# Optimization experiments

Measured on AMD Instinct MI355X. Metric: run time of the kernel, lower is better.

## Reference

```python
import jax, jax.numpy as jnp
import numpy as np

B, S, E, H = 4, 2048, 1024, 16
D = E // H  # head_dim = 64
ROPE_BASE = 10000.0


def _rope(x):
    # x: [B, H, S, D] -> rotary position embedding applied over seq dim
    seq_len = x.shape[2]
    inv_freq = 1.0 / (ROPE_BASE ** (jnp.arange(0, D, 2, dtype=jnp.float32) / D))  # [D/2]
    freqs = jnp.arange(seq_len, dtype=jnp.float32)[:, None] * inv_freq[None, :]   # [S, D/2]
    emb = jnp.concatenate([freqs, freqs], axis=-1)                                 # [S, D]
    cos = jnp.cos(emb).astype(x.dtype)
    sin = jnp.sin(emb).astype(x.dtype)
    x1, x2 = jnp.split(x, 2, axis=-1)
    rotated = jnp.concatenate([-x2, x1], axis=-1)
    return x * cos + rotated * sin


def setup_inputs() -> dict:
    key = jax.random.key(0)
    ks = jax.random.split(key, 10)
    p = 0.02
    return {
        "x": jax.random.normal(ks[0], (B, S, E), dtype=jnp.float32),
        "Wq": jax.random.normal(ks[1], (E, E), dtype=jnp.float32) * p,
        "bq": jnp.zeros((E,), dtype=jnp.float32),
        "Wk": jax.random.normal(ks[2], (E, E), dtype=jnp.float32) * p,
        "bk": jnp.zeros((E,), dtype=jnp.float32),
        "Wv": jax.random.normal(ks[3], (E, E), dtype=jnp.float32) * p,
        "bv": jnp.zeros((E,), dtype=jnp.float32),
        "Wo": jax.random.normal(ks[4], (E, E), dtype=jnp.float32) * p,
        "bo": jnp.zeros((E,), dtype=jnp.float32),
        "key_padding_mask": jnp.zeros((B, S), dtype=bool),
    }


def reference(x, Wq, bq, Wk, bk, Wv, bv, Wo, bo, key_padding_mask):
    b, s, _ = x.shape
    # QKV projections -> [B, H, S, D]
    def proj(W, bias):
        return (x @ W + bias).reshape(b, s, H, D).transpose(0, 2, 1, 3)
    q = _rope(proj(Wq, bq))
    k = _rope(proj(Wk, bk))
    v = proj(Wv, bv)
    scale = D ** -0.5
    scores = jnp.einsum('bhqd,bhkd->bhqk', q, k) * scale  # [B, H, S, S]
    scores = jnp.where(key_padding_mask[:, None, None, :], jnp.finfo(scores.dtype).min, scores)
    probs = jax.nn.softmax(scores, axis=-1)
    out = jnp.einsum('bhqk,bhkd->bhqd', probs, v)         # [B, H, S, D]
    out = out.transpose(0, 2, 1, 3).reshape(b, s, E)
    return out @ Wo + bo
```

## Files before the change

### kernel.cpp

```cpp
#include <hip/hip_runtime.h>
#include <hip/hip_bf16.h>
#include <math.h>

#define Bn 4
#define Sn 2048
#define En 1024
#define Hn 16
#define Dn 64
#define Mn (Bn * Sn)

typedef __attribute__((ext_vector_type(8))) short short8;
typedef __attribute__((ext_vector_type(4))) short short4v;
typedef __attribute__((ext_vector_type(4))) float f32x4;
typedef __attribute__((ext_vector_type(16))) float f32x16;
typedef __attribute__((ext_vector_type(2))) unsigned int uint2v;

#if __has_builtin(__builtin_amdgcn_exp2f)
#define EXP2(x) __builtin_amdgcn_exp2f(x)
#else
#define EXP2(x) exp2f(x)
#endif

#if __has_builtin(__builtin_amdgcn_permlane32_swap)
#define HAVE_PLSWAP 1
#endif

#define GLOAD16(g, s) __builtin_amdgcn_global_load_lds( \
    (const __attribute__((address_space(1))) unsigned int*)(g), \
    (__attribute__((address_space(3))) unsigned int*)(s), 16, 0, 0)

__device__ inline unsigned short f2bf(float f) {
    unsigned int u = __float_as_uint(f);
    u += 0x7FFFu + ((u >> 16) & 1u);
    return (unsigned short)(u >> 16);
}
__device__ inline float bf2f(unsigned short h) {
    return __uint_as_float(((unsigned int)h) << 16);
}
__device__ inline short8 ld8s(const unsigned short* p) {
    union { short4v h[2]; short8 v; } r;
    r.h[0] = *(const short4v*)p;
    r.h[1] = *(const short4v*)(p + 4);
    return r.v;
}
__device__ inline short8 g8(const unsigned short* p) {
    union { int4 i; short8 v; } r;
    r.i = *(const int4*)p;
    return r.v;
}

__device__ inline void st16(unsigned short* base, int row, int col16, int4 v) {
    const unsigned off = ((unsigned)(row * 128 + col16 * 2)) ^ ((unsigned)((row & 7) << 4));
    *(int4*)((char*)base + off) = v;
}
__device__ inline short8 ld16(const unsigned short* base, int row, int col16) {
    const unsigned off = ((unsigned)(row * 128 + col16 * 2)) ^ ((unsigned)((row & 7) << 4));
    union { int4 i; short8 v; } r;
    r.i = *(const int4*)((const char*)base + off);
    return r.v;
}

__global__ __launch_bounds__(256) void prep_kernel(
    const float* __restrict__ X, unsigned short* __restrict__ Xh,
    const float* __restrict__ Wq, const float* __restrict__ Wk,
    const float* __restrict__ Wv, const float* __restrict__ Wo,
    unsigned short* __restrict__ WqkvT, unsigned short* __restrict__ WoT,
    float* __restrict__ ct, float* __restrict__ st) {
    const int m = blockIdx.z;
    const int t = threadIdx.x;
    if (m >= 5) {
        const int i = ((m - 5) * 256 + blockIdx.y * 16 + blockIdx.x) * 256 + t;
        float4 v = ((const float4*)X)[i];
        float f[4] = {v.x, v.y, v.z, v.w};
        short4v h;
#pragma unroll
        for (int j = 0; j < 4; ++j) h[j] = (short)f2bf(f[j]);
        ((short4v*)Xh)[i] = h;
        return;
    }
    if (m == 4) {
        const int i = (blockIdx.y * 16 + blockIdx.x) * 256 + t;
        const int s = i >> 5, p = i & 31;
        double inv = pow(10000.0, -(double)p / 32.0);
        double a = (double)s * inv;
        ct[i] = (float)cos(a);
        st[i] = (float)sin(a);
        return;
    }
    const float* W = (m == 0) ? Wq : (m == 1) ? Wk : (m == 2) ? Wv : Wo;
    unsigned short* dst = (m < 3) ? WqkvT + (size_t)m * En * En : WoT;

    __shared__ float Ws[64][65];
    const int kb = blockIdx.y * 64, nb = blockIdx.x * 64;
    const int lr = t >> 2, lc = (t & 3) * 16;
#pragma unroll
    for (int u = 0; u < 4; ++u) {
        float4 v = *(const float4*)&W[(size_t)(kb + lr) * En + nb + lc + 4 * u];
        Ws[lr][lc + 4 * u + 0] = v.x; Ws[lr][lc + 4 * u + 1] = v.y;
        Ws[lr][lc + 4 * u + 2] = v.z; Ws[lr][lc + 4 * u + 3] = v.w;
    }
    __syncthreads();
    const int orow = t >> 2, ock = (t & 3) * 16;
#pragma unroll
    for (int u = 0; u < 4; ++u) {
        short4v hs;
#pragma unroll
        for (int j = 0; j < 4; ++j) hs[j] = (short)f2bf(Ws[ock + 4 * u + j][orow]);
        *(short4v*)&dst[(size_t)(nb + orow) * En + kb + ock + 4 * u] = hs;
    }
}

template <int KN>
__global__ __launch_bounds__(256, 4) void gemm97(
    const unsigned short* __restrict__ A, const unsigned short* __restrict__ Bt,
    const float* __restrict__ b0, const float* __restrict__ bkv,
    const float* __restrict__ bvv,
    unsigned short* __restrict__ oQ, unsigned short* __restrict__ oK,
    unsigned short* __restrict__ oV,
    const float* __restrict__ ct, const float* __restrict__ st) {
    __shared__ __align__(16) unsigned short shmem[17408];
    unsigned short (*As)[64] = (unsigned short(*)[64])&shmem[0];
    unsigned short (*Bs)[64] = (unsigned short(*)[64])&shmem[8192];
    const int t = threadIdx.x;
    const int w = t >> 6, l = t & 63;
    const int wm = w & 1, wn = w >> 1;
    const int q = l >> 4, ln16 = l & 15;
    const int r8 = l >> 3, i8 = l & 7;

    int bx = blockIdx.x, by = blockIdx.y;
    {
        const int gx = gridDim.x;
        const int nwg = gx * gridDim.y;
        if ((nwg & 7) == 0) {
            const int n = by * gx + bx;
            const int s = (n & 7) * (nwg >> 3) + (n >> 3);
            bx = s % gx; by = s / gx;
        }
    }
    const int m0 = by * 128, n0 = bx * 128;

    f32x4 acc[4][4];
#pragma unroll
    for (int i = 0; i < 4; ++i)
#pragma unroll
        for (int j = 0; j < 4; ++j)
#pragma unroll
            for (int r = 0; r < 4; ++r) acc[i][j][r] = 0.0f;

    const unsigned short* Ag = &A[(size_t)(m0 + 32 * w + r8) * KN + 8 * i8];
    const unsigned short* Bg = &Bt[(size_t)(n0 + 32 * w + r8) * KN + 8 * i8];

    for (int k0 = 0; k0 < KN; k0 += 64) {
        __syncthreads();
#pragma unroll
        for (int j = 0; j < 4; ++j) {
            GLOAD16(Ag + (size_t)(8 * j) * KN + k0, &As[32 * w + 8 * j][0]);
            GLOAD16(Bg + (size_t)(8 * j) * KN + k0, &Bs[32 * w + 8 * j][0]);
        }
        __syncthreads();
#pragma unroll
        for (int ks = 0; ks < 2; ++ks) {
            short8 af[4], bf[4];
#pragma unroll
            for (int i = 0; i < 4; ++i)
                af[i] = ld8s(&As[64 * wm + 16 * i + ln16][32 * ks + 8 * q]);
#pragma unroll
            for (int j = 0; j < 4; ++j)
                bf[j] = ld8s(&Bs[64 * wn + 16 * j + ln16][32 * ks + 8 * q]);
#pragma unroll
            for (int i = 0; i < 4; ++i)
#pragma unroll
                for (int j = 0; j < 4; ++j)
                    acc[i][j] = __builtin_amdgcn_mfma_f32_16x16x32_bf16(
                        af[i], bf[j], acc[i][j], 0, 0, 0);
        }
    }

    const int mat = n0 >> 10;
    const int nIn0 = n0 & 1023;
    if (mat == 2) {
        __syncthreads();
#pragma unroll
        for (int i = 0; i < 4; ++i)
#pragma unroll
            for (int j = 0; j < 4; ++j) {
                const int dl = 64 * wn + 16 * j + ln16;
                const float bv2 = bvv[nIn0 + dl];
#pragma unroll
                for (int r = 0; r < 4; ++r) {
                    const int sl = 64 * wm + 16 * i + 4 * q + r;
                    shmem[dl * 136 + sl] = f2bf(acc[i][j][r] + bv2);
                }
            }
        __syncthreads();
        const int dr2 = t >> 1, sc2 = (t & 1) * 64;
        const int hh2 = (nIn0 >> 6) + (dr2 >> 6);
        unsigned short* vp =
            &oV[(((size_t)((m0 >> 11) * Hn + hh2)) * Dn + (dr2 & 63)) * Sn
                + (m0 & (Sn - 1)) + sc2];
        const unsigned short* tp = &shmem[dr2 * 136 + sc2];
#pragma unroll
        for (int u = 0; u < 8; ++u)
            *(int4*)(vp + 8 * u) = *(const int4*)(tp + 8 * u);
    } else {
        const int nIn = nIn0 + 64 * wn;
        const int hh = nIn >> 6;
        const float* bias = (mat == 0) ? b0 : bkv;
        unsigned short* op = (mat == 0) ? oQ : oK;
#pragma unroll
        for (int i = 0; i < 4; ++i)
#pragma unroll
            for (int r = 0; r < 4; ++r) {
                const int m = m0 + 64 * wm + 16 * i + 4 * q + r;
                const int b = m >> 11, s2 = m & (Sn - 1);
                const size_t base = (((size_t)(b * Hn + hh)) * Sn + s2) * Dn;
#pragma unroll
                for (int j = 0; j < 2; ++j) {
                    const int nh = 16 * j + ln16;
                    float v0 = acc[i][j][r] + bias[nIn + nh];
                    float v1 = acc[i][j + 2][r] + bias[nIn + nh + 32];
                    float c = ct[s2 * 32 + nh], sn = st[s2 * 32 + nh];
                    float o0 = v0 * c - v1 * sn;
                    float o1 = v1 * c + v0 * sn;
                    if (mat == 0) {
                        o0 *= 0.18033688011112042f;
                        o1 *= 0.18033688011112042f;
                    }
                    op[base + nh] = f2bf(o0);
                    op[base + nh + 32] = f2bf(o1);
                }
            }
    }
}

__global__ __launch_bounds__(128, 4) void gemm64o(
    const unsigned short* __restrict__ A, const unsigned short* __restrict__ Bt,
    const float* __restrict__ b0, float* __restrict__ oF) {
    __shared__ unsigned short As[64][64];
    __shared__ unsigned short Bs[128][64];
    const int t = threadIdx.x;
    const int w = t >> 6, l = t & 63;
    const int q = l >> 4, ln16 = l & 15;
    const int r8 = l >> 3, i8 = l & 7;

    int bx = blockIdx.x, by = blockIdx.y;
    {
        const int gx = gridDim.x;
        const int nwg = gx * gridDim.y;
        const int n = by * gx + bx;
        const int s = (n & 7) * (nwg >> 3) + (n >> 3);
        bx = s % gx; by = s / gx;
    }
    const int m0 = by * 64, n0 = bx * 128;

    f32x4 acc[4][4];
#pragma unroll
    for (int i = 0; i < 4; ++i)
#pragma unroll
        for (int j = 0; j < 4; ++j)
#pragma unroll
            for (int r = 0; r < 4; ++r) acc[i][j][r] = 0.0f;

    const unsigned short* Ag = &A[(size_t)(m0 + 32 * w + r8) * En + 8 * i8];
    const unsigned short* Bg = &Bt[(size_t)(n0 + 64 * w + r8) * En + 8 * i8];

    for (int k0 = 0; k0 < En; k0 += 64) {
        __syncthreads();
#pragma unroll
        for (int j = 0; j < 4; ++j)
            GLOAD16(Ag + (size_t)(8 * j) * En + k0, &As[32 * w + 8 * j][0]);
#pragma unroll
        for (int j = 0; j < 8; ++j)
            GLOAD16(Bg + (size_t)(8 * j) * En + k0, &Bs[64 * w + 8 * j][0]);
        __syncthreads();
#pragma unroll
        for (int ks = 0; ks < 2; ++ks) {
            short8 af[4], bf[4];
#pragma unroll
            for (int i = 0; i < 4; ++i)
                af[i] = ld8s(&As[16 * i + ln16][32 * ks + 8 * q]);
#pragma unroll
            for (int j = 0; j < 4; ++j)
                bf[j] = ld8s(&Bs[64 * w + 16 * j + ln16][32 * ks + 8 * q]);
#pragma unroll
            for (int i = 0; i < 4; ++i)
#pragma unroll
                for (int j = 0; j < 4; ++j)
                    acc[i][j] = __builtin_amdgcn_mfma_f32_16x16x32_bf16(
                        af[i], bf[j], acc[i][j], 0, 0, 0);
        }
    }

#pragma unroll
    for (int i = 0; i < 4; ++i)
#pragma unroll
        for (int r = 0; r < 4; ++r) {
            const int m = m0 + 16 * i + 4 * q + r;
#pragma unroll
            for (int j = 0; j < 4; ++j) {
                const int n = n0 + 64 * w + 16 * j + ln16;
                oF[(size_t)m * En + n] = acc[i][j][r] + b0[n];
            }
        }
}

__device__ inline void softpack(const f32x16& accS, unsigned long long bm,
                                int c, int h2, float* lsum, unsigned* pw) {
#pragma unroll
    for (int g = 0; g < 4; ++g)
#pragma unroll
        for (int j = 0; j < 2; ++j) {
            const int r0 = 4 * g + 2 * j;
            float p0 = EXP2(accS[r0]);
            float p1 = EXP2(accS[r0 + 1]);
            if (bm) {
                const int key = 32 * c + 8 * g + 4 * h2 + 2 * j;
                if ((bm >> key) & 1) p0 = 0.0f;
                if ((bm >> (key + 1)) & 1) p1 = 0.0f;
            }
            const unsigned u0 = __float_as_uint(p0) & 0xFFFF0000u;
            const unsigned u1 = __float_as_uint(p1) & 0xFFFF0000u;
            lsum[g] += __uint_as_float(u0);
            lsum[g] += __uint_as_float(u1);
            pw[2 * g + j] = (u0 >> 16) | u1;
        }
}

__device__ inline short8 pv_afrag(const unsigned* pw, int s, int h2) {
    union { unsigned u[4]; short8 v; } af;
#ifdef HAVE_PLSWAP
    uint2v r02 = __builtin_amdgcn_permlane32_swap(
        pw[4 * s + 0], pw[4 * s + 2], false, false);
    uint2v r13 = __builtin_amdgcn_permlane32_swap(
        pw[4 * s + 1], pw[4 * s + 3], false, false);
    af.u[0] = r02[0]; af.u[1] = r13[0];
    af.u[2] = r02[1]; af.u[3] = r13[1];
#else
    const unsigned x0 = pw[4 * s + 0], x1 = pw[4 * s + 1];
    const unsigned y0 = pw[4 * s + 2], y1 = pw[4 * s + 3];
    const unsigned py0 = (unsigned)__shfl_xor((int)y0, 32);
    const unsigned py1 = (unsigned)__shfl_xor((int)y1, 32);
    const unsigned px0 = (unsigned)__shfl_xor((int)x0, 32);
    const unsigned px1 = (unsigned)__shfl_xor((int)x1, 32);
    af.u[0] = h2 ? py0 : x0;
    af.u[1] = h2 ? py1 : x1;
    af.u[2] = h2 ? y0 : px0;
    af.u[3] = h2 ? y1 : px1;
#endif
    return af.v;
}

__global__ __launch_bounds__(256) void attn_mfma_kernel(
    const unsigned short* __restrict__ Qb, const unsigned short* __restrict__ Kb,
    const unsigned short* __restrict__ VbT, const unsigned char* __restrict__ mask,
    unsigned short* __restrict__ Obuf) {
    __shared__ __align__(16) unsigned short Ks[2][64][64];
    __shared__ __align__(16) unsigned short Vs[2][64][64];

    const int t = threadIdx.x;
    const int w = t >> 6, l = t & 63, h2 = l >> 5, ln = l & 31;

    int qt, h, b;
    {
        const int n = blockIdx.x + 16 * (blockIdx.y + 16 * blockIdx.z);
        const int w2 = ((n & 7) << 7) + (n >> 3);
        qt = w2 & 15; h = (w2 >> 4) & 15; b = w2 >> 8;
    }
    const int q0 = qt * 128;
    const size_t ho = ((size_t)(b * Hn + h)) * Sn * Dn;
    const unsigned char* maskB = mask + (size_t)b * Sn;

    short8 qh[4];
    const int qrow = q0 + 32 * w + ln;
#pragma unroll
    for (int s = 0; s < 4; ++s)
        qh[s] = g8(&Qb[ho + (size_t)qrow * Dn + 16 * s + 8 * h2]);

    f32x16 accO0, accO1;
#pragma unroll
    for (int i = 0; i < 16; ++i) { accO0[i] = 0.0f; accO1[i] = 0.0f; }
    float lsum[4] = {0.0f, 0.0f, 0.0f, 0.0f};

    const int kr = t >> 2, kc = (t & 3) * 16;
    const unsigned short* Kp = &Kb[ho + (size_t)kr * Dn + kc];
    const unsigned short* Vp = &VbT[ho + (size_t)kr * Sn + kc];

    int4 ck0 = *(const int4*)Kp, ck1 = *(const int4*)(Kp + 8);
    int4 cv0 = *(const int4*)Vp, cv1 = *(const int4*)(Vp + 8);
    unsigned char cm = maskB[l];

#pragma unroll 2
    for (int kt = 0; kt < Sn / 64; ++kt) {
        const int pb = kt & 1;
        unsigned short* KsP = &Ks[pb][0][0];
        unsigned short* VsP = &Vs[pb][0][0];
        st16(KsP, kr, kc, ck0); st16(KsP, kr, kc + 8, ck1);
        st16(VsP, kr, kc, cv0); st16(VsP, kr, kc + 8, cv1);
        const unsigned long long bm = __ballot(cm != 0);
        __syncthreads();
        const int kn = ((kt + 1) & (Sn / 64 - 1)) * 64;
        ck0 = *(const int4*)(Kp + (size_t)kn * Dn);
        ck1 = *(const int4*)(Kp + (size_t)kn * Dn + 8);
        cv0 = *(const int4*)(Vp + kn);
        cv1 = *(const int4*)(Vp + kn + 8);
        cm = maskB[kn + l];

#pragma unroll
        for (int c = 0; c < 2; ++c) {
            short8 kf[4];
#pragma unroll
            for (int s = 0; s < 4; ++s)
                kf[s] = ld16(KsP, 32 * c + ln, 16 * s + 8 * h2);
            f32x16 accS;
#pragma unroll
            for (int i = 0; i < 16; ++i) accS[i] = 0.0f;
            __builtin_amdgcn_s_setprio(1);
#pragma unroll
            for (int s = 0; s < 4; ++s)
                accS = __builtin_amdgcn_mfma_f32_32x32x16_bf16(kf[s], qh[s], accS, 0, 0, 0);
            __builtin_amdgcn_s_setprio(0);

            unsigned pw[8];
            softpack(accS, bm, c, h2, lsum, pw);

#pragma unroll
            for (int s = 0; s < 2; ++s) {
                short8 af = pv_afrag(pw, s, h2);
                short8 vA = ld16(VsP, ln, 32 * c + 16 * s + 8 * h2);
                short8 vB = ld16(VsP, 32 + ln, 32 * c + 16 * s + 8 * h2);
                __builtin_amdgcn_s_setprio(1);
                accO0 = __builtin_amdgcn_mfma_f32_32x32x16_bf16(af, vA, accO0, 0, 0, 0);
                accO1 = __builtin_amdgcn_mfma_f32_32x32x16_bf16(af, vB, accO1, 0, 0, 0);
                __builtin_amdgcn_s_setprio(0);
            }
        }
    }

    const float lme = (lsum[0] + lsum[1]) + (lsum[2] + lsum[3]);
    const float tot = lme + __shfl_xor(lme, 32);
    const float linv = 1.0f / fmaxf(tot, 1e-37f);
#pragma unroll
    for (int r = 0; r < 16; ++r) {
        const int row = (r & 3) + 8 * (r >> 2) + 4 * h2;
        const float lr = __shfl(linv, row);
        const int s = q0 + 32 * w + row;
        const size_t base = ((size_t)b * Sn + s) * 1024 + h * Dn;
        Obuf[base + ln] = f2bf(accO0[r] * lr);
        Obuf[base + 32 + ln] = f2bf(accO1[r] * lr);
    }
}

extern "C" void kernel_launch(void* const* d_in, const int* in_sizes, int n_in,
                              void* d_out, int out_size, void* d_ws, size_t ws_size,
                              hipStream_t stream) {
    const float* x  = (const float*)d_in[0];
    const float* Wq = (const float*)d_in[1];
    const float* bq = (const float*)d_in[2];
    const float* Wk = (const float*)d_in[3];
    const float* bk = (const float*)d_in[4];
    const float* Wv = (const float*)d_in[5];
    const float* bv = (const float*)d_in[6];
    const float* Wo = (const float*)d_in[7];
    const float* bo = (const float*)d_in[8];
    const unsigned char* mask = (const unsigned char*)d_in[9];

    const size_t NE = (size_t)Mn * En;
    const size_t WN = (size_t)En * En;
    unsigned short* ws = (unsigned short*)d_ws;
    unsigned short* Xh = ws;
    unsigned short* Qb = Xh + NE;
    unsigned short* Kb = Qb + NE;
    unsigned short* VbT = Kb + NE;
    unsigned short* Obuf = VbT + NE;
    unsigned short* WqkvT = Obuf + NE;
    unsigned short* WoT = WqkvT + 3 * WN;
    float* ct = (float*)(WoT + WN);
    float* st = ct + (size_t)Sn * 32;

    prep_kernel<<<dim3(16, 16, 37), 256, 0, stream>>>(
        x, Xh, Wq, Wk, Wv, Wo, WqkvT, WoT, ct, st);

    gemm97<En><<<dim3(3 * En / 128, Mn / 128), 256, 0, stream>>>(
        Xh, WqkvT, bq, bk, bv, Qb, Kb, VbT, ct, st);

    attn_mfma_kernel<<<dim3(Sn / 128, Hn, Bn), 256, 0, stream>>>(
        Qb, Kb, VbT, mask, Obuf);

    gemm64o<<<dim3(En / 128, Mn / 64), 128, 0, stream>>>(
        Obuf, WoT, bo, (float*)d_out);
}
```

Baseline: 298.7 us.

## Rewrite QKV GEMM as 256x256 tile, 8-wave double-buffered ping-pong pipeline

```diff
diff --git a/kernel.cpp b/kernel.cpp
--- a/kernel.cpp
+++ b/kernel.cpp
@@ -111,19 +111,20 @@
 }
 
 template <int KN>
-__global__ __launch_bounds__(256, 4) void gemm97(
+__global__ __launch_bounds__(512, 2) void gemm8p(
     const unsigned short* __restrict__ A, const unsigned short* __restrict__ Bt,
     const float* __restrict__ b0, const float* __restrict__ bkv,
     const float* __restrict__ bvv,
     unsigned short* __restrict__ oQ, unsigned short* __restrict__ oK,
     unsigned short* __restrict__ oV,
     const float* __restrict__ ct, const float* __restrict__ st) {
-    __shared__ __align__(16) unsigned short shmem[17408];
-    unsigned short (*As)[64] = (unsigned short(*)[64])&shmem[0];
-    unsigned short (*Bs)[64] = (unsigned short(*)[64])&shmem[8192];
+    __shared__ __align__(16) unsigned short shmem[67584];
+    unsigned short (*As)[256][64] = (unsigned short(*)[256][64])&shmem[0];
+    unsigned short (*Bs)[256][64] = (unsigned short(*)[256][64])&shmem[32768];
+
     const int t = threadIdx.x;
     const int w = t >> 6, l = t & 63;
-    const int wm = w & 1, wn = w >> 1;
+    const int wm = w >> 2, wn = w & 3;
     const int q = l >> 4, ln16 = l & 15;
     const int r8 = l >> 3, i8 = l & 7;
 
@@ -131,76 +132,161 @@
     {
         const int gx = gridDim.x;
         const int nwg = gx * gridDim.y;
-        if ((nwg & 7) == 0) {
-            const int n = by * gx + bx;
-            const int s = (n & 7) * (nwg >> 3) + (n >> 3);
-            bx = s % gx; by = s / gx;
-        }
-    }
-    const int m0 = by * 128, n0 = bx * 128;
-
-    f32x4 acc[4][4];
-#pragma unroll
-    for (int i = 0; i < 4; ++i)
+        const int n = by * gx + bx;
+        const int s = (n & 7) * (nwg >> 3) + (n >> 3);
+        bx = s % gx; by = s / gx;
+    }
+    const int m0 = by * 256, n0 = bx * 256;
+
+    f32x4 acc[8][4];
+#pragma unroll
+    for (int i = 0; i < 8; ++i)
 #pragma unroll
         for (int j = 0; j < 4; ++j)
 #pragma unroll
             for (int r = 0; r < 4; ++r) acc[i][j][r] = 0.0f;
 
-    const unsigned short* Ag = &A[(size_t)(m0 + 32 * w + r8) * KN + 8 * i8];
-    const unsigned short* Bg = &Bt[(size_t)(n0 + 32 * w + r8) * KN + 8 * i8];
-
-    for (int k0 = 0; k0 < KN; k0 += 64) {
-        __syncthreads();
-#pragma unroll
-        for (int j = 0; j < 4; ++j) {
-            GLOAD16(Ag + (size_t)(8 * j) * KN + k0, &As[32 * w + 8 * j][0]);
-            GLOAD16(Bg + (size_t)(8 * j) * KN + k0, &Bs[32 * w + 8 * j][0]);
-        }
-        __syncthreads();
-#pragma unroll
-        for (int ks = 0; ks < 2; ++ks) {
-            short8 af[4], bf[4];
-#pragma unroll
-            for (int i = 0; i < 4; ++i)
-                af[i] = ld8s(&As[64 * wm + 16 * i + ln16][32 * ks + 8 * q]);
-#pragma unroll
-            for (int j = 0; j < 4; ++j)
-                bf[j] = ld8s(&Bs[64 * wn + 16 * j + ln16][32 * ks + 8 * q]);
-#pragma unroll
-            for (int i = 0; i < 4; ++i)
-#pragma unroll
-                for (int j = 0; j < 4; ++j)
+    const unsigned short* Ag = &A[(size_t)(m0 + 16 * w + r8) * KN + 8 * i8];
+    const unsigned short* Bg = &Bt[(size_t)(n0 + 16 * w + r8) * KN + 8 * i8];
+
+#define STAGE_A8(buf, k0g) do { \
+    GLOAD16(Ag + (k0g),                  &As[buf][16 * w][0]); \
+    GLOAD16(Ag + (size_t)8 * KN + (k0g), &As[buf][16 * w + 8][0]); \
+    GLOAD16(Ag + (size_t)128 * KN + (k0g), &As[buf][128 + 16 * w][0]); \
+    GLOAD16(Ag + (size_t)136 * KN + (k0g), &As[buf][128 + 16 * w + 8][0]); \
+} while (0)
+#define STAGE_B8L(buf, k0g) do { \
+    GLOAD16(Bg + (k0g),                  &Bs[buf][16 * w][0]); \
+    GLOAD16(Bg + (size_t)8 * KN + (k0g), &Bs[buf][16 * w + 8][0]); \
+} while (0)
+#define STAGE_B8H(buf, k0g) do { \
+    GLOAD16(Bg + (size_t)128 * KN + (k0g), &Bs[buf][128 + 16 * w][0]); \
+    GLOAD16(Bg + (size_t)136 * KN + (k0g), &Bs[buf][128 + 16 * w + 8][0]); \
+} while (0)
+
+    STAGE_A8(0, 0);
+    STAGE_B8L(0, 0);
+    STAGE_B8H(0, 0);
+    asm volatile("s_waitcnt vmcnt(0)" ::: "memory");
+    __builtin_amdgcn_s_barrier();
+
+    short8 af[8], bf0[4], bf1[4];
+    for (int kt = 0; kt < KN / 64; ++kt) {
+        const int cur = kt & 1, nxt = cur ^ 1;
+        const size_t kn1 = (size_t)(kt + 1) * 64;
+        const bool more = (kt + 1 < KN / 64);
+
+#pragma unroll
+        for (int ks = 0; ks < 2; ++ks)
+#pragma unroll
+            for (int i = 0; i < 4; ++i)
+                af[4 * ks + i] = ld8s(&As[cur][128 * wm + 16 * i + ln16][32 * ks + 8 * q]);
+#pragma unroll
+        for (int ks = 0; ks < 2; ++ks)
+#pragma unroll
+            for (int j = 0; j < 2; ++j)
+                bf0[2 * ks + j] = ld8s(&Bs[cur][64 * wn + 16 * j + ln16][32 * ks + 8 * q]);
+        if (more) STAGE_A8(nxt, kn1);
+        __builtin_amdgcn_s_barrier();
+        asm volatile("s_waitcnt lgkmcnt(0)" ::: "memory");
+        __builtin_amdgcn_sched_barrier(0);
+        __builtin_amdgcn_s_setprio(1);
+#pragma unroll
+        for (int ks = 0; ks < 2; ++ks)
+#pragma unroll
+            for (int i = 0; i < 4; ++i)
+#pragma unroll
+                for (int j = 0; j < 2; ++j)
                     acc[i][j] = __builtin_amdgcn_mfma_f32_16x16x32_bf16(
-                        af[i], bf[j], acc[i][j], 0, 0, 0);
-        }
-    }
+                        af[4 * ks + i], bf0[2 * ks + j], acc[i][j], 0, 0, 0);
+        __builtin_amdgcn_s_setprio(0);
+        __builtin_amdgcn_s_barrier();
+
+#pragma unroll
+        for (int ks = 0; ks < 2; ++ks)
+#pragma unroll
+            for (int j = 0; j < 2; ++j)
+                bf1[2 * ks + j] = ld8s(&Bs[cur][64 * wn + 32 + 16 * j + ln16][32 * ks + 8 * q]);
+        if (more) STAGE_B8L(nxt, kn1);
+        __builtin_amdgcn_s_barrier();
+        asm volatile("s_waitcnt lgkmcnt(0)" ::: "memory");
+        __builtin_amdgcn_sched_barrier(0);
+        __builtin_amdgcn_s_setprio(1);
+#pragma unroll
+        for (int ks = 0; ks < 2; ++ks)
+#pragma unroll
+            for (int i = 0; i < 4; ++i)
+#pragma unroll
+                for (int j = 0; j < 2; ++j)
+                    acc[i][2 + j] = __builtin_amdgcn_mfma_f32_16x16x32_bf16(
+                        af[4 * ks + i], bf1[2 * ks + j], acc[i][2 + j], 0, 0, 0);
+        __builtin_amdgcn_s_setprio(0);
+        __builtin_amdgcn_s_barrier();
+
+#pragma unroll
+        for (int ks = 0; ks < 2; ++ks)
+#pragma unroll
+            for (int i = 0; i < 4; ++i)
+                af[4 * ks + i] = ld8s(&As[cur][128 * wm + 64 + 16 * i + ln16][32 * ks + 8 * q]);
+        if (more) STAGE_B8H(nxt, kn1);
+        __builtin_amdgcn_s_barrier();
+        asm volatile("s_waitcnt lgkmcnt(0)" ::: "memory");
+        __builtin_amdgcn_sched_barrier(0);
+        __builtin_amdgcn_s_setprio(1);
+#pragma unroll
+        for (int ks = 0; ks < 2; ++ks)
+#pragma unroll
+            for (int i = 0; i < 4; ++i)
+#pragma unroll
+                for (int j = 0; j < 2; ++j)
+                    acc[4 + i][j] = __builtin_amdgcn_mfma_f32_16x16x32_bf16(
+                        af[4 * ks + i], bf0[2 * ks + j], acc[4 + i][j], 0, 0, 0);
+        __builtin_amdgcn_s_setprio(0);
+        __builtin_amdgcn_s_barrier();
+
+        asm volatile("s_waitcnt vmcnt(0)" ::: "memory");
+        __builtin_amdgcn_s_barrier();
+        __builtin_amdgcn_s_setprio(1);
+#pragma unroll
+        for (int ks = 0; ks < 2; ++ks)
+#pragma unroll
+            for (int i = 0; i < 4; ++i)
+#pragma unroll
+                for (int j = 0; j < 2; ++j)
+                    acc[4 + i][2 + j] = __builtin_amdgcn_mfma_f32_16x16x32_bf16(
+                        af[4 * ks + i], bf1[2 * ks + j], acc[4 + i][2 + j], 0, 0, 0);
+        __builtin_amdgcn_s_setprio(0);
+        __builtin_amdgcn_s_barrier();
+    }
+#undef STAGE_A8
+#undef STAGE_B8L
+#undef STAGE_B8H
 
     const int mat = n0 >> 10;
     const int nIn0 = n0 & 1023;
     if (mat == 2) {
         __syncthreads();
 #pragma unroll
-        for (int i = 0; i < 4; ++i)
+        for (int i = 0; i < 8; ++i)
 #pragma unroll
             for (int j = 0; j < 4; ++j) {
                 const int dl = 64 * wn + 16 * j + ln16;
                 const float bv2 = bvv[nIn0 + dl];
 #pragma unroll
                 for (int r = 0; r < 4; ++r) {
-                    const int sl = 64 * wm + 16 * i + 4 * q + r;
-                    shmem[dl * 136 + sl] = f2bf(acc[i][j][r] + bv2);
+                    const int sl = 128 * wm + 16 * i + 4 * q + r;
+                    shmem[dl * 264 + sl] = f2bf(acc[i][j][r] + bv2);
                 }
             }
         __syncthreads();
-        const int dr2 = t >> 1, sc2 = (t & 1) * 64;
+        const int dr2 = t >> 1, sc2 = (t & 1) * 128;
         const int hh2 = (nIn0 >> 6) + (dr2 >> 6);
         unsigned short* vp =
             &oV[(((size_t)((m0 >> 11) * Hn + hh2)) * Dn + (dr2 & 63)) * Sn
                 + (m0 & (Sn - 1)) + sc2];
-        const unsigned short* tp = &shmem[dr2 * 136 + sc2];
-#pragma unroll
-        for (int u = 0; u < 8; ++u)
+        const unsigned short* tp = &shmem[dr2 * 264 + sc2];
+#pragma unroll
+        for (int u = 0; u < 16; ++u)
             *(int4*)(vp + 8 * u) = *(const int4*)(tp + 8 * u);
     } else {
         const int nIn = nIn0 + 64 * wn;
@@ -208,10 +294,10 @@
         const float* bias = (mat == 0) ? b0 : bkv;
         unsigned short* op = (mat == 0) ? oQ : oK;
 #pragma unroll
-        for (int i = 0; i < 4; ++i)
+        for (int i = 0; i < 8; ++i)
 #pragma unroll
             for (int r = 0; r < 4; ++r) {
-                const int m = m0 + 64 * wm + 16 * i + 4 * q + r;
+                const int m = m0 + 128 * wm + 16 * i + 4 * q + r;
                 const int b = m >> 11, s2 = m & (Sn - 1);
                 const size_t base = (((size_t)(b * Hn + hh)) * Sn + s2) * Dn;
 #pragma unroll
@@ -480,7 +566,7 @@
     prep_kernel<<<dim3(16, 16, 37), 256, 0, stream>>>(
         x, Xh, Wq, Wk, Wv, Wo, WqkvT, WoT, ct, st);
 
-    gemm97<En><<<dim3(3 * En / 128, Mn / 128), 256, 0, stream>>>(
+    gemm8p<En><<<dim3(3 * En / 256, Mn / 256), 512, 0, stream>>>(
         Xh, WqkvT, bq, bk, bv, Qb, Kb, VbT, ct, st);
 
     attn_mfma_kernel<<<dim3(Sn / 128, Hn, Bn), 256, 0, stream>>>(
```

After: 365.6 us. +22.4%, slower.
